# Performance work log

Hardware: AMD Instinct MI355X
Metric: run time of the kernel (lower is better)

## Reference

```python
import jax, jax.numpy as jnp
import numpy as np

B, C, H, W = 16, 256, 64, 64
NH, WS = 8, 8  # num_heads, window_size
HD = C // NH   # head_dim = 32


def setup_inputs() -> dict:
    key = jax.random.key(0)
    k1, k2, k3 = jax.random.split(key, 3)
    x = jax.random.normal(k1, (B, C, H, W), dtype=jnp.float32)
    w_qkv = jax.random.normal(k2, (3 * C, C), dtype=jnp.float32) * 0.02  # 1x1 conv, no bias
    w_proj = jax.random.normal(k3, (C, C), dtype=jnp.float32) * 0.02
    return {"x": x, "w_qkv": w_qkv, "w_proj": w_proj, "shift": 1}


def _window_partition(t, ws):
    # [b,c,h,w] -> [b*(h/ws)*(w/ws), ws*ws, c]
    b, c, h, w = t.shape
    t = t.reshape(b, c, h // ws, ws, w // ws, ws)
    t = t.transpose(0, 2, 4, 3, 5, 1)
    return t.reshape(-1, ws * ws, c)


def _window_reverse(t, b, c, h, w, ws):
    t = t.reshape(b, h // ws, w // ws, ws, ws, c)
    t = t.transpose(0, 5, 1, 3, 2, 4)
    return t.reshape(b, c, h, w)


def reference(x, w_qkv, w_proj, shift):
    b, c, h, w = x.shape
    ws = min(WS, h, w)
    shift_size = ws // 2 if (shift and ws > 1 and h % ws == 0 and w % ws == 0) else 0
    if shift_size > 0:
        x = jnp.roll(x, (-shift_size, -shift_size), axis=(2, 3))
    # 1x1 conv QKV: [b,c,h,w] x [3c,c] -> [b,3c,h,w]
    qkv = jnp.einsum('bchw,oc->bohw', x, w_qkv)
    q, k, v = jnp.split(qkv, 3, axis=1)
    q_t = _window_partition(q, ws)  # [Bw, S, c], S = ws*ws
    k_t = _window_partition(k, ws)
    v_t = _window_partition(v, ws)
    bw, s, _ = q_t.shape
    # heads: [Bw, nh, S, hd]
    qh = q_t.reshape(bw, s, NH, HD).transpose(0, 2, 1, 3)
    kh = k_t.reshape(bw, s, NH, HD).transpose(0, 2, 1, 3)
    vh = v_t.reshape(bw, s, NH, HD).transpose(0, 2, 1, 3)
    scale = 1.0 / jnp.sqrt(jnp.asarray(HD, dtype=qh.dtype))
    scores = jnp.einsum('bnqd,bnkd->bnqk', qh, kh) * scale
    attn = jax.nn.softmax(scores, axis=-1)
    out = jnp.einsum('bnqk,bnkd->bnqd', attn, vh)
    out = out.transpose(0, 2, 1, 3).reshape(bw, s, c)
    out = _window_reverse(out, b, c, h, w, ws)
    if shift_size > 0:
        out = jnp.roll(out, (shift_size, shift_size), axis=(2, 3))
    return jnp.einsum('bchw,oc->bohw', out, w_proj)
```

## Files before the change

kernel.cpp:

```cpp
#include <hip/hip_runtime.h>

typedef short bf16x8 __attribute__((ext_vector_type(8)));
typedef float f32x4 __attribute__((ext_vector_type(4)));
typedef unsigned short u16;
typedef unsigned int u32;

static __device__ __forceinline__ u16 f2bf(float f) {
  u32 u = __builtin_bit_cast(u32, f);
  u32 r = (u + 0x7FFFu + ((u >> 16) & 1u)) >> 16;
  return (u16)r;
}

__global__ __launch_bounds__(256) void k_conv(
    const float* __restrict__ wqkv, const float* __restrict__ wproj,
    u16* __restrict__ wbf) {
  const int cid = blockIdx.x * 256 + threadIdx.x;
  const float* src;
  int dst;
  if (cid < 24576) {
    const int tile = cid >> 9, rem = cid & 511;
    const int k = rem >> 6, lane = rem & 63;
    src = wqkv + (size_t)(tile * 16 + (lane & 15)) * 256 + k * 32 + (lane >> 4) * 8;
    dst = cid;
  } else {
    const int pid = cid - 24576;
    const int mt = pid >> 9, rem = pid & 511;
    const int h = rem >> 6, lane = rem & 63;
    src = wproj + (size_t)(mt * 16 + (lane & 15)) * 256 + h * 32 + (lane >> 4) * 8;
    dst = 24576 + h * 1024 + mt * 64 + lane;
  }
  float4 f0 = *(const float4*)(src);
  float4 f1 = *(const float4*)(src + 4);
  ushort4 a, b;
  a.x = f2bf(f0.x); a.y = f2bf(f0.y); a.z = f2bf(f0.z); a.w = f2bf(f0.w);
  b.x = f2bf(f1.x); b.y = f2bf(f1.y); b.z = f2bf(f1.z); b.w = f2bf(f1.w);
  *(ushort4*)(wbf + (size_t)dst * 8) = a;
  *(ushort4*)(wbf + (size_t)dst * 8 + 4) = b;
}

#define BUF0 0
#define BUF1 4096
#define XB 0
#define QH 8192
#define KH 10752
#define VTH 13312
#define PH 15616
#define LDS_TOT 20224

#define MEMF() asm volatile("" ::: "memory")
#define ENTRY()                                                      \
  do {                                                               \
    asm volatile("s_waitcnt vmcnt(0) lgkmcnt(0)" ::: "memory");      \
    __builtin_amdgcn_s_barrier();                                    \
    MEMF();                                                          \
  } while (0)

#define GL2LDS(gp, lp)                                   \
  __builtin_amdgcn_global_load_lds(                      \
      (__attribute__((address_space(1))) void*)(gp),     \
      (__attribute__((address_space(3))) void*)(lp), 16, 0, 0)

static __device__ __forceinline__ void stage_half(const u16* g, u16* l, int t) {
#pragma unroll
  for (int j = 0; j < 2; ++j) {
    const int off = (j * 256 + t) * 8;
    GL2LDS(g + off, l + off);
  }
}

#define QKV_TILE(BUFB, DSTB, U)                                           \
  do {                                                                    \
    const u16* wb_ = LDS + (BUFB) + lane * 8;                             \
    f32x4 acc = {0.f, 0.f, 0.f, 0.f};                                     \
    _Pragma("unroll") for (int k = 0; k < 8; ++k) acc =                   \
        __builtin_amdgcn_mfma_f32_16x16x32_bf16(                          \
            af[k], *(const bf16x8*)(wb_ + k * 512), acc, 0, 0, 0);        \
    _Pragma("unroll") for (int r = 0; r < 4; ++r)                         \
        LDS[(DSTB) + (pos0 + r) * 40 + (U) * 16 + l15] = f2bf(acc[r]);    \
  } while (0)

#define V_TILE(BUFB, U)                                                   \
  do {                                                                    \
    const u16* wb_ = LDS + (BUFB) + lane * 8;                             \
    f32x4 acc = {0.f, 0.f, 0.f, 0.f};                                     \
    _Pragma("unroll") for (int k = 0; k < 8; ++k) acc =                   \
        __builtin_amdgcn_mfma_f32_16x16x32_bf16(                          \
            af[k], *(const bf16x8*)(wb_ + k * 512), acc, 0, 0, 0);        \
    ushort4 pk;                                                           \
    pk.x = f2bf(acc[0]); pk.y = f2bf(acc[1]);                             \
    pk.z = f2bf(acc[2]); pk.w = f2bf(acc[3]);                             \
    *(ushort4*)&LDS[VTH + ((U) * 16 + l15) * 72 + pos0] = pk;             \
  } while (0)

__global__ __launch_bounds__(256, 4) void k_fused(
    const float* __restrict__ x, const u16* __restrict__ wbf,
    const int* __restrict__ shiftp, float* __restrict__ out) {
  __shared__ u16 LDS[LDS_TOT];
  const int blk = blockIdx.x;
  const int win = ((blk & 127) << 3) | (blk >> 7);
  const int b = win >> 6, wh = (win >> 3) & 7, ww = win & 7;
  const int off = (shiftp[0] != 0) ? 4 : 0;
  const int t = threadIdx.x;

  {
    const int slot = (blk >> 8) & 3;
    if (slot == 1) __builtin_amdgcn_s_sleep(16);
    else if (slot == 2) __builtin_amdgcn_s_sleep(32);
    else if (slot == 3) __builtin_amdgcn_s_sleep(48);
  }

  {
    u16* X = LDS + XB;
    const int wr = t & 7;
    const int h = ((wh << 3) + wr + off) & 63;
    const int w0 = ((ww << 3) + off) & 63;
    const int w1 = ((ww << 3) + off + 4) & 63;
    const int p0 = wr << 3;
#pragma unroll
    for (int it = 0; it < 8; ++it) {
      const int c = (t >> 3) + (it << 5);
      const float* src = x + ((size_t)(b * 256 + c) * 64 + h) * 64;
      float4 v0 = *(const float4*)(src + w0);
      float4 v1 = *(const float4*)(src + w1);
      X[(p0 + 0) * 264 + c] = f2bf(v0.x);
      X[(p0 + 1) * 264 + c] = f2bf(v0.y);
      X[(p0 + 2) * 264 + c] = f2bf(v0.z);
      X[(p0 + 3) * 264 + c] = f2bf(v0.w);
      X[(p0 + 4) * 264 + c] = f2bf(v1.x);
      X[(p0 + 5) * 264 + c] = f2bf(v1.y);
      X[(p0 + 6) * 264 + c] = f2bf(v1.z);
      X[(p0 + 7) * 264 + c] = f2bf(v1.w);
    }
  }
  __syncthreads();

  const int lane = t & 63, wv = t >> 6;
  const int l15 = lane & 15, quad = lane >> 4;
  const int pos0 = wv * 16 + quad * 4;

  bf16x8 af[8];
#pragma unroll
  for (int k = 0; k < 8; ++k)
    af[k] = *(const bf16x8*)&LDS[XB + (wv * 16 + l15) * 264 + quad * 8 + k * 32];
  asm volatile("s_waitcnt lgkmcnt(0)" ::: "memory");
  __builtin_amdgcn_s_barrier();
  MEMF();

  stage_half(wbf, LDS + BUF0, t);

  f32x4 accP[16];
#pragma unroll
  for (int mt = 0; mt < 16; ++mt) accP[mt] = (f32x4){0.f, 0.f, 0.f, 0.f};

  const float scale = 0.17677669529663687f;
  u16* Pw = LDS + PH + wv * 1152;
  bf16x8 bo;

#pragma unroll 1
  for (int h = 0; h < 8; ++h) {
    ENTRY();
    stage_half(wbf + (size_t)(h * 2 + 1) * 4096, LDS + BUF1, t);
    QKV_TILE(BUF0, QH, 0);
    ENTRY();
    stage_half(wbf + (size_t)(16 + h * 2) * 4096, LDS + BUF0, t);
    QKV_TILE(BUF1, QH, 1);
    ENTRY();
    stage_half(wbf + (size_t)(17 + h * 2) * 4096, LDS + BUF1, t);
    QKV_TILE(BUF0, KH, 0);
    ENTRY();
    stage_half(wbf + (size_t)(32 + h * 2) * 4096, LDS + BUF0, t);
    QKV_TILE(BUF1, KH, 1);
    ENTRY();
    stage_half(wbf + (size_t)(33 + h * 2) * 4096, LDS + BUF1, t);
    V_TILE(BUF0, 0);
    ENTRY();
    stage_half(wbf + 196608 + (size_t)h * 8192, LDS + BUF0, t);
    V_TILE(BUF1, 1);
    ENTRY();
    stage_half(wbf + 196608 + (size_t)h * 8192 + 4096, LDS + BUF1, t);
    {
      bf16x8 aq = *(const bf16x8*)&LDS[QH + (wv * 16 + l15) * 40 + quad * 8];
      f32x4 sc[4];
#pragma unroll
      for (int nt = 0; nt < 4; ++nt) {
        bf16x8 bk = *(const bf16x8*)&LDS[KH + (nt * 16 + l15) * 40 + quad * 8];
        f32x4 z = {0.f, 0.f, 0.f, 0.f};
        sc[nt] = __builtin_amdgcn_mfma_f32_16x16x32_bf16(aq, bk, z, 0, 0, 0);
      }
#pragma unroll
      for (int r = 0; r < 4; ++r) {
        float mx = -1e30f;
#pragma unroll
        for (int nt = 0; nt < 4; ++nt) mx = fmaxf(mx, sc[nt][r]);
        mx = fmaxf(mx, __shfl_xor(mx, 1));
        mx = fmaxf(mx, __shfl_xor(mx, 2));
        mx = fmaxf(mx, __shfl_xor(mx, 4));
        mx = fmaxf(mx, __shfl_xor(mx, 8));
        float p[4], sum = 0.f;
#pragma unroll
        for (int nt = 0; nt < 4; ++nt) {
          p[nt] = __expf((sc[nt][r] - mx) * scale);
          sum += p[nt];
        }
        sum += __shfl_xor(sum, 1);
        sum += __shfl_xor(sum, 2);
        sum += __shfl_xor(sum, 4);
        sum += __shfl_xor(sum, 8);
        const float is = 1.f / sum;
#pragma unroll
        for (int nt = 0; nt < 4; ++nt)
          Pw[(quad * 4 + r) * 72 + nt * 16 + l15] = f2bf(p[nt] * is);
      }
      f32x4 oa[2];
      oa[0] = (f32x4){0.f, 0.f, 0.f, 0.f};
      oa[1] = (f32x4){0.f, 0.f, 0.f, 0.f};
#pragma unroll
      for (int kk = 0; kk < 2; ++kk) {
        bf16x8 ap = *(const bf16x8*)&Pw[l15 * 72 + kk * 32 + quad * 8];
#pragma unroll
        for (int n2 = 0; n2 < 2; ++n2) {
          bf16x8 bv =
              *(const bf16x8*)&LDS[VTH + (n2 * 16 + l15) * 72 + kk * 32 + quad * 8];
          oa[n2] = __builtin_amdgcn_mfma_f32_16x16x32_bf16(ap, bv, oa[n2], 0, 0, 0);
        }
      }
#pragma unroll
      for (int n2 = 0; n2 < 2; ++n2)
#pragma unroll
        for (int r = 0; r < 4; ++r)
          LDS[QH + (pos0 + r) * 40 + n2 * 16 + l15] = f2bf(oa[n2][r]);
      bo = *(const bf16x8*)&LDS[QH + (wv * 16 + l15) * 40 + quad * 8];
#pragma unroll
      for (int mt = 0; mt < 8; ++mt) {
        bf16x8 aw = *(const bf16x8*)&LDS[BUF0 + mt * 512 + lane * 8];
        accP[mt] = __builtin_amdgcn_mfma_f32_16x16x32_bf16(aw, bo, accP[mt], 0, 0, 0);
      }
    }
    ENTRY();
    if (h < 7)
      stage_half(wbf + (size_t)((h + 1) * 2) * 4096, LDS + BUF0, t);
#pragma unroll
    for (int mt = 0; mt < 8; ++mt) {
      bf16x8 aw = *(const bf16x8*)&LDS[BUF1 + mt * 512 + lane * 8];
      accP[8 + mt] =
          __builtin_amdgcn_mfma_f32_16x16x32_bf16(aw, bo, accP[8 + mt], 0, 0, 0);
    }
  }

  const int pos = wv * 16 + l15;
  const int hco = ((wh << 3) + (pos >> 3) + off) & 63;
  const int wco = ((ww << 3) + (pos & 7) + off) & 63;
#pragma unroll
  for (int mt = 0; mt < 16; ++mt)
#pragma unroll
    for (int r = 0; r < 4; ++r) {
      const int c = mt * 16 + quad * 4 + r;
      out[((size_t)(b * 256 + c) << 12) + (hco << 6) + wco] = accP[mt][r];
    }
}

extern "C" void kernel_launch(void* const* d_in, const int* in_sizes, int n_in,
                              void* d_out, int out_size, void* d_ws, size_t ws_size,
                              hipStream_t stream) {
  const float* x = (const float*)d_in[0];
  const float* wqkv = (const float*)d_in[1];
  const float* wproj = (const float*)d_in[2];
  const int* shiftp = (const int*)d_in[3];
  float* outp = (float*)d_out;
  u16* wbf = (u16*)d_ws;
  hipLaunchKernelGGL(k_conv, dim3(128), dim3(256), 0, stream, wqkv, wproj, wbf);
  hipLaunchKernelGGL(k_fused, dim3(1024), dim3(256), 0, stream, x, wbf, shiftp, outp);
}
```

Measured before the change: 222.4 us.

## Process two windows per 512-thread block to share staged weight tiles

```diff
diff --git a/kernel.cpp b/kernel.cpp
--- a/kernel.cpp
+++ b/kernel.cpp
@@ -40,12 +40,12 @@
 
 #define BUF0 0
 #define BUF1 4096
-#define XB 0
-#define QH 8192
-#define KH 10752
-#define VTH 13312
-#define PH 15616
-#define LDS_TOT 20224
+#define ATT_BASE 8192
+#define ATT_STRIDE 12032
+#define KH_OFF 2560
+#define VTH_OFF 5120
+#define P_OFF 7424
+#define LDS_TOT 32256
 
 #define MEMF() asm volatile("" ::: "memory")
 #define ENTRY()                                                      \
@@ -60,12 +60,8 @@
       (__attribute__((address_space(1))) void*)(gp),     \
       (__attribute__((address_space(3))) void*)(lp), 16, 0, 0)
 
-static __device__ __forceinline__ void stage_half(const u16* g, u16* l, int t) {
-#pragma unroll
-  for (int j = 0; j < 2; ++j) {
-    const int off = (j * 256 + t) * 8;
-    GL2LDS(g + off, l + off);
-  }
+static __device__ __forceinline__ void stage1(const u16* g, u16* l, int t) {
+  GL2LDS(g + t * 8, l + t * 8);
 }
 
 #define QKV_TILE(BUFB, DSTB, U)                                           \
@@ -89,101 +85,105 @@
     ushort4 pk;                                                           \
     pk.x = f2bf(acc[0]); pk.y = f2bf(acc[1]);                             \
     pk.z = f2bf(acc[2]); pk.w = f2bf(acc[3]);                             \
-    *(ushort4*)&LDS[VTH + ((U) * 16 + l15) * 72 + pos0] = pk;             \
+    *(ushort4*)&LDS[VTHs + ((U) * 16 + l15) * 72 + pos0] = pk;            \
   } while (0)
 
-__global__ __launch_bounds__(256, 4) void k_fused(
+__global__ __launch_bounds__(512, 4) void k_fused(
     const float* __restrict__ x, const u16* __restrict__ wbf,
     const int* __restrict__ shiftp, float* __restrict__ out) {
   __shared__ u16 LDS[LDS_TOT];
   const int blk = blockIdx.x;
-  const int win = ((blk & 127) << 3) | (blk >> 7);
-  const int b = win >> 6, wh = (win >> 3) & 7, ww = win & 7;
+  const int pair = ((blk & 127) << 2) | (blk >> 7);
+  const int b = pair >> 5, wh = (pair >> 2) & 7, wwp = pair & 3;
   const int off = (shiftp[0] != 0) ? 4 : 0;
   const int t = threadIdx.x;
-
-  {
-    const int slot = (blk >> 8) & 3;
-    if (slot == 1) __builtin_amdgcn_s_sleep(16);
-    else if (slot == 2) __builtin_amdgcn_s_sleep(32);
-    else if (slot == 3) __builtin_amdgcn_s_sleep(48);
-  }
-
-  {
-    u16* X = LDS + XB;
-    const int wr = t & 7;
-    const int h = ((wh << 3) + wr + off) & 63;
-    const int w0 = ((ww << 3) + off) & 63;
-    const int w1 = ((ww << 3) + off + 4) & 63;
-    const int p0 = wr << 3;
-#pragma unroll
-    for (int it = 0; it < 8; ++it) {
-      const int c = (t >> 3) + (it << 5);
-      const float* src = x + ((size_t)(b * 256 + c) * 64 + h) * 64;
-      float4 v0 = *(const float4*)(src + w0);
-      float4 v1 = *(const float4*)(src + w1);
-      X[(p0 + 0) * 264 + c] = f2bf(v0.x);
-      X[(p0 + 1) * 264 + c] = f2bf(v0.y);
-      X[(p0 + 2) * 264 + c] = f2bf(v0.z);
-      X[(p0 + 3) * 264 + c] = f2bf(v0.w);
-      X[(p0 + 4) * 264 + c] = f2bf(v1.x);
-      X[(p0 + 5) * 264 + c] = f2bf(v1.y);
-      X[(p0 + 6) * 264 + c] = f2bf(v1.z);
-      X[(p0 + 7) * 264 + c] = f2bf(v1.w);
-    }
-  }
-  __syncthreads();
-
-  const int lane = t & 63, wv = t >> 6;
+  const int side = t >> 8;
+  const int ww = wwp * 2 + side;
+
+  if ((blk >> 8) & 1) __builtin_amdgcn_s_sleep(24);
+
+  const int lane = t & 63, wv = (t >> 6) & 3;
   const int l15 = lane & 15, quad = lane >> 4;
   const int pos0 = wv * 16 + quad * 4;
 
   bf16x8 af[8];
-#pragma unroll
-  for (int k = 0; k < 8; ++k)
-    af[k] = *(const bf16x8*)&LDS[XB + (wv * 16 + l15) * 264 + quad * 8 + k * 32];
-  asm volatile("s_waitcnt lgkmcnt(0)" ::: "memory");
-  __builtin_amdgcn_s_barrier();
-  MEMF();
-
-  stage_half(wbf, LDS + BUF0, t);
+#pragma unroll 1
+  for (int s = 0; s < 2; ++s) {
+    {
+      u16* X = LDS;
+      const int wr = t & 7;
+      const int h = ((wh << 3) + wr + off) & 63;
+      const int wx = wwp * 2 + s;
+      const int w0 = ((wx << 3) + off) & 63;
+      const int w1 = ((wx << 3) + off + 4) & 63;
+      const int p0 = wr << 3;
+#pragma unroll
+      for (int it = 0; it < 4; ++it) {
+        const int c = (t >> 3) + (it << 6);
+        const float* src = x + ((size_t)(b * 256 + c) * 64 + h) * 64;
+        float4 v0 = *(const float4*)(src + w0);
+        float4 v1 = *(const float4*)(src + w1);
+        X[(p0 + 0) * 264 + c] = f2bf(v0.x);
+        X[(p0 + 1) * 264 + c] = f2bf(v0.y);
+        X[(p0 + 2) * 264 + c] = f2bf(v0.z);
+        X[(p0 + 3) * 264 + c] = f2bf(v0.w);
+        X[(p0 + 4) * 264 + c] = f2bf(v1.x);
+        X[(p0 + 5) * 264 + c] = f2bf(v1.y);
+        X[(p0 + 6) * 264 + c] = f2bf(v1.z);
+        X[(p0 + 7) * 264 + c] = f2bf(v1.w);
+      }
+    }
+    __syncthreads();
+    if (side == s) {
+#pragma unroll
+      for (int k = 0; k < 8; ++k)
+        af[k] = *(const bf16x8*)&LDS[(wv * 16 + l15) * 264 + quad * 8 + k * 32];
+    }
+    asm volatile("s_waitcnt lgkmcnt(0)" ::: "memory");
+    __syncthreads();
+  }
+
+  stage1(wbf, LDS + BUF0, t);
+
+  const int AT = ATT_BASE + side * ATT_STRIDE;
+  const int QHs = AT, KHs = AT + KH_OFF, VTHs = AT + VTH_OFF;
+  u16* Pw = LDS + AT + P_OFF + wv * 1152;
 
   f32x4 accP[16];
 #pragma unroll
   for (int mt = 0; mt < 16; ++mt) accP[mt] = (f32x4){0.f, 0.f, 0.f, 0.f};
 
   const float scale = 0.17677669529663687f;
-  u16* Pw = LDS + PH + wv * 1152;
   bf16x8 bo;
 
 #pragma unroll 1
   for (int h = 0; h < 8; ++h) {
     ENTRY();
-    stage_half(wbf + (size_t)(h * 2 + 1) * 4096, LDS + BUF1, t);
-    QKV_TILE(BUF0, QH, 0);
-    ENTRY();
-    stage_half(wbf + (size_t)(16 + h * 2) * 4096, LDS + BUF0, t);
-    QKV_TILE(BUF1, QH, 1);
-    ENTRY();
-    stage_half(wbf + (size_t)(17 + h * 2) * 4096, LDS + BUF1, t);
-    QKV_TILE(BUF0, KH, 0);
-    ENTRY();
-    stage_half(wbf + (size_t)(32 + h * 2) * 4096, LDS + BUF0, t);
-    QKV_TILE(BUF1, KH, 1);
-    ENTRY();
-    stage_half(wbf + (size_t)(33 + h * 2) * 4096, LDS + BUF1, t);
+    stage1(wbf + (size_t)(h * 2 + 1) * 4096, LDS + BUF1, t);
+    QKV_TILE(BUF0, QHs, 0);
+    ENTRY();
+    stage1(wbf + (size_t)(16 + h * 2) * 4096, LDS + BUF0, t);
+    QKV_TILE(BUF1, QHs, 1);
+    ENTRY();
+    stage1(wbf + (size_t)(17 + h * 2) * 4096, LDS + BUF1, t);
+    QKV_TILE(BUF0, KHs, 0);
+    ENTRY();
+    stage1(wbf + (size_t)(32 + h * 2) * 4096, LDS + BUF0, t);
+    QKV_TILE(BUF1, KHs, 1);
+    ENTRY();
+    stage1(wbf + (size_t)(33 + h * 2) * 4096, LDS + BUF1, t);
     V_TILE(BUF0, 0);
     ENTRY();
-    stage_half(wbf + 196608 + (size_t)h * 8192, LDS + BUF0, t);
+    stage1(wbf + 196608 + (size_t)h * 8192, LDS + BUF0, t);
     V_TILE(BUF1, 1);
     ENTRY();
-    stage_half(wbf + 196608 + (size_t)h * 8192 + 4096, LDS + BUF1, t);
+    stage1(wbf + 196608 + (size_t)h * 8192 + 4096, LDS + BUF1, t);
     {
-      bf16x8 aq = *(const bf16x8*)&LDS[QH + (wv * 16 + l15) * 40 + quad * 8];
+      bf16x8 aq = *(const bf16x8*)&LDS[QHs + (wv * 16 + l15) * 40 + quad * 8];
       f32x4 sc[4];
 #pragma unroll
       for (int nt = 0; nt < 4; ++nt) {
-        bf16x8 bk = *(const bf16x8*)&LDS[KH + (nt * 16 + l15) * 40 + quad * 8];
+        bf16x8 bk = *(const bf16x8*)&LDS[KHs + (nt * 16 + l15) * 40 + quad * 8];
         f32x4 z = {0.f, 0.f, 0.f, 0.f};
         sc[nt] = __builtin_amdgcn_mfma_f32_16x16x32_bf16(aq, bk, z, 0, 0, 0);
       }
@@ -220,7 +220,7 @@
 #pragma unroll
         for (int n2 = 0; n2 < 2; ++n2) {
           bf16x8 bv =
-              *(const bf16x8*)&LDS[VTH + (n2 * 16 + l15) * 72 + kk * 32 + quad * 8];
+              *(const bf16x8*)&LDS[VTHs + (n2 * 16 + l15) * 72 + kk * 32 + quad * 8];
           oa[n2] = __builtin_amdgcn_mfma_f32_16x16x32_bf16(ap, bv, oa[n2], 0, 0, 0);
         }
       }
@@ -228,8 +228,8 @@
       for (int n2 = 0; n2 < 2; ++n2)
 #pragma unroll
         for (int r = 0; r < 4; ++r)
-          LDS[QH + (pos0 + r) * 40 + n2 * 16 + l15] = f2bf(oa[n2][r]);
-      bo = *(const bf16x8*)&LDS[QH + (wv * 16 + l15) * 40 + quad * 8];
+          LDS[QHs + (pos0 + r) * 40 + n2 * 16 + l15] = f2bf(oa[n2][r]);
+      bo = *(const bf16x8*)&LDS[QHs + (wv * 16 + l15) * 40 + quad * 8];
 #pragma unroll
       for (int mt = 0; mt < 8; ++mt) {
         bf16x8 aw = *(const bf16x8*)&LDS[BUF0 + mt * 512 + lane * 8];
@@ -238,7 +238,7 @@
     }
     ENTRY();
     if (h < 7)
-      stage_half(wbf + (size_t)((h + 1) * 2) * 4096, LDS + BUF0, t);
+      stage1(wbf + (size_t)((h + 1) * 2) * 4096, LDS + BUF0, t);
 #pragma unroll
     for (int mt = 0; mt < 8; ++mt) {
       bf16x8 aw = *(const bf16x8*)&LDS[BUF1 + mt * 512 + lane * 8];
@@ -269,5 +269,5 @@
   float* outp = (float*)d_out;
   u16* wbf = (u16*)d_ws;
   hipLaunchKernelGGL(k_conv, dim3(128), dim3(256), 0, stream, wqkv, wproj, wbf);
-  hipLaunchKernelGGL(k_fused, dim3(1024), dim3(256), 0, stream, x, wbf, shiftp, outp);
-}
+  hipLaunchKernelGGL(k_fused, dim3(512), dim3(512), 0, stream, x, wbf, shiftp, outp);
+}
```

New measurement: 228.9 us. 1.03x slower.

## Split QKV and projection GEMMs across wave pairs with 4-buffer weight staging

Applied to the files above, without the earlier changes.

```diff
diff --git a/kernel.cpp b/kernel.cpp
--- a/kernel.cpp
+++ b/kernel.cpp
@@ -38,22 +38,30 @@
   *(ushort4*)(wbf + (size_t)dst * 8 + 4) = b;
 }
 
-#define BUF0 0
-#define BUF1 4096
-#define XB 0
-#define QH 8192
-#define KH 10752
-#define VTH 13312
-#define PH 15616
-#define LDS_TOT 20224
+#define B0 0
+#define B1 4096
+#define B2 8192
+#define B3 12288
+#define QH 16384
+#define KH 18944
+#define VTH 21504
+#define PH 23808
+#define LDS_TOT 28416
 
 #define MEMF() asm volatile("" ::: "memory")
+#define BAR()                        \
+  do {                               \
+    MEMF();                          \
+    __builtin_amdgcn_s_barrier();    \
+    MEMF();                          \
+  } while (0)
 #define ENTRY()                                                      \
   do {                                                               \
     asm volatile("s_waitcnt vmcnt(0) lgkmcnt(0)" ::: "memory");      \
     __builtin_amdgcn_s_barrier();                                    \
     MEMF();                                                          \
   } while (0)
+#define WLG0() asm volatile("s_waitcnt lgkmcnt(0)" ::: "memory")
 
 #define GL2LDS(gp, lp)                                   \
   __builtin_amdgcn_global_load_lds(                      \
@@ -68,31 +76,43 @@
   }
 }
 
-#define QKV_TILE(BUFB, DSTB, U)                                           \
-  do {                                                                    \
-    const u16* wb_ = LDS + (BUFB) + lane * 8;                             \
-    f32x4 acc = {0.f, 0.f, 0.f, 0.f};                                     \
-    _Pragma("unroll") for (int k = 0; k < 8; ++k) acc =                   \
-        __builtin_amdgcn_mfma_f32_16x16x32_bf16(                          \
-            af[k], *(const bf16x8*)(wb_ + k * 512), acc, 0, 0, 0);        \
-    _Pragma("unroll") for (int r = 0; r < 4; ++r)                         \
-        LDS[(DSTB) + (pos0 + r) * 40 + (U) * 16 + l15] = f2bf(acc[r]);    \
+#define GEMM_TILE(BUFB, DSTB, U)                                              \
+  do {                                                                        \
+    const u16* wb_ = LDS + (BUFB) + lane * 8;                                 \
+    f32x4 a0 = {0.f, 0.f, 0.f, 0.f}, a1 = {0.f, 0.f, 0.f, 0.f};               \
+    _Pragma("unroll") for (int k = 0; k < 8; ++k) {                           \
+      const bf16x8 bf_ = *(const bf16x8*)(wb_ + k * 512);                     \
+      a0 = __builtin_amdgcn_mfma_f32_16x16x32_bf16(af0[k], bf_, a0, 0, 0, 0); \
+      a1 = __builtin_amdgcn_mfma_f32_16x16x32_bf16(af1[k], bf_, a1, 0, 0, 0); \
+    }                                                                         \
+    _Pragma("unroll") for (int r = 0; r < 4; ++r) {                           \
+      LDS[(DSTB) + (wp * 32 + quad * 4 + r) * 40 + (U) * 16 + l15] =          \
+          f2bf(a0[r]);                                                        \
+      LDS[(DSTB) + (wp * 32 + 16 + quad * 4 + r) * 40 + (U) * 16 + l15] =     \
+          f2bf(a1[r]);                                                        \
+    }                                                                         \
   } while (0)
 
-#define V_TILE(BUFB, U)                                                   \
-  do {                                                                    \
-    const u16* wb_ = LDS + (BUFB) + lane * 8;                             \
-    f32x4 acc = {0.f, 0.f, 0.f, 0.f};                                     \
-    _Pragma("unroll") for (int k = 0; k < 8; ++k) acc =                   \
-        __builtin_amdgcn_mfma_f32_16x16x32_bf16(                          \
-            af[k], *(const bf16x8*)(wb_ + k * 512), acc, 0, 0, 0);        \
-    ushort4 pk;                                                           \
-    pk.x = f2bf(acc[0]); pk.y = f2bf(acc[1]);                             \
-    pk.z = f2bf(acc[2]); pk.w = f2bf(acc[3]);                             \
-    *(ushort4*)&LDS[VTH + ((U) * 16 + l15) * 72 + pos0] = pk;             \
+#define VGEMM_TILE(BUFB, U)                                                   \
+  do {                                                                        \
+    const u16* wb_ = LDS + (BUFB) + lane * 8;                                 \
+    f32x4 a0 = {0.f, 0.f, 0.f, 0.f}, a1 = {0.f, 0.f, 0.f, 0.f};               \
+    _Pragma("unroll") for (int k = 0; k < 8; ++k) {                           \
+      const bf16x8 bf_ = *(const bf16x8*)(wb_ + k * 512);                     \
+      a0 = __builtin_amdgcn_mfma_f32_16x16x32_bf16(af0[k], bf_, a0, 0, 0, 0); \
+      a1 = __builtin_amdgcn_mfma_f32_16x16x32_bf16(af1[k], bf_, a1, 0, 0, 0); \
+    }                                                                         \
+    ushort4 pk0, pk1;                                                         \
+    pk0.x = f2bf(a0[0]); pk0.y = f2bf(a0[1]);                                 \
+    pk0.z = f2bf(a0[2]); pk0.w = f2bf(a0[3]);                                 \
+    pk1.x = f2bf(a1[0]); pk1.y = f2bf(a1[1]);                                 \
+    pk1.z = f2bf(a1[2]); pk1.w = f2bf(a1[3]);                                 \
+    *(ushort4*)&LDS[VTH + ((U) * 16 + l15) * 72 + wp * 32 + quad * 4] = pk0;  \
+    *(ushort4*)&LDS[VTH + ((U) * 16 + l15) * 72 + wp * 32 + 16 + quad * 4] =  \
+        pk1;                                                                  \
   } while (0)
 
-__global__ __launch_bounds__(256, 4) void k_fused(
+__global__ __launch_bounds__(256, 2) void k_fused(
     const float* __restrict__ x, const u16* __restrict__ wbf,
     const int* __restrict__ shiftp, float* __restrict__ out) {
   __shared__ u16 LDS[LDS_TOT];
@@ -110,7 +130,7 @@
   }
 
   {
-    u16* X = LDS + XB;
+    u16* X = LDS;
     const int wr = t & 7;
     const int h = ((wh << 3) + wr + off) & 63;
     const int w0 = ((ww << 3) + off) & 63;
@@ -136,48 +156,54 @@
 
   const int lane = t & 63, wv = t >> 6;
   const int l15 = lane & 15, quad = lane >> 4;
-  const int pos0 = wv * 16 + quad * 4;
-
-  bf16x8 af[8];
-#pragma unroll
-  for (int k = 0; k < 8; ++k)
-    af[k] = *(const bf16x8*)&LDS[XB + (wv * 16 + l15) * 264 + quad * 8 + k * 32];
-  asm volatile("s_waitcnt lgkmcnt(0)" ::: "memory");
-  __builtin_amdgcn_s_barrier();
-  MEMF();
-
-  stage_half(wbf, LDS + BUF0, t);
-
-  f32x4 accP[16];
-#pragma unroll
-  for (int mt = 0; mt < 16; ++mt) accP[mt] = (f32x4){0.f, 0.f, 0.f, 0.f};
+  const int wp = wv >> 1, wc = wv & 1;
+  const int apos0 = wv * 16 + quad * 4;
+
+  bf16x8 af0[8], af1[8];
+#pragma unroll
+  for (int k = 0; k < 8; ++k) {
+    af0[k] = *(const bf16x8*)&LDS[(wp * 32 + l15) * 264 + quad * 8 + k * 32];
+    af1[k] =
+        *(const bf16x8*)&LDS[(wp * 32 + 16 + l15) * 264 + quad * 8 + k * 32];
+  }
+  WLG0();
+  BAR();
+
+  stage_half(wbf, LDS + B0, t);
+  stage_half(wbf + (size_t)17 * 4096, LDS + B1, t);
+
+  f32x4 accP[8][2];
+#pragma unroll
+  for (int mt = 0; mt < 8; ++mt) {
+    accP[mt][0] = (f32x4){0.f, 0.f, 0.f, 0.f};
+    accP[mt][1] = (f32x4){0.f, 0.f, 0.f, 0.f};
+  }
 
   const float scale = 0.17677669529663687f;
   u16* Pw = LDS + PH + wv * 1152;
-  bf16x8 bo;
 
 #pragma unroll 1
   for (int h = 0; h < 8; ++h) {
     ENTRY();
-    stage_half(wbf + (size_t)(h * 2 + 1) * 4096, LDS + BUF1, t);
-    QKV_TILE(BUF0, QH, 0);
+    stage_half(wbf + (size_t)(h * 2 + 1) * 4096, LDS + B2, t);
+    stage_half(wbf + (size_t)(32 + h * 2) * 4096, LDS + B3, t);
+    if (wc == 0) GEMM_TILE(B0, QH, 0);
+    else GEMM_TILE(B1, KH, 1);
     ENTRY();
-    stage_half(wbf + (size_t)(16 + h * 2) * 4096, LDS + BUF0, t);
-    QKV_TILE(BUF1, QH, 1);
+    stage_half(wbf + (size_t)(16 + h * 2) * 4096, LDS + B0, t);
+    stage_half(wbf + (size_t)(33 + h * 2) * 4096, LDS + B1, t);
+    if (wc == 0) GEMM_TILE(B2, QH, 1);
+    else VGEMM_TILE(B3, 0);
     ENTRY();
-    stage_half(wbf + (size_t)(17 + h * 2) * 4096, LDS + BUF1, t);
-    QKV_TILE(BUF0, KH, 0);
+    stage_half(wbf + 196608 + (size_t)h * 8192, LDS + B2, t);
+    stage_half(wbf + 196608 + (size_t)h * 8192 + 4096, LDS + B3, t);
+    if (wc == 0) GEMM_TILE(B0, KH, 0);
+    else VGEMM_TILE(B1, 1);
     ENTRY();
-    stage_half(wbf + (size_t)(32 + h * 2) * 4096, LDS + BUF0, t);
-    QKV_TILE(BUF1, KH, 1);
-    ENTRY();
-    stage_half(wbf + (size_t)(33 + h * 2) * 4096, LDS + BUF1, t);
-    V_TILE(BUF0, 0);
-    ENTRY();
-    stage_half(wbf + 196608 + (size_t)h * 8192, LDS + BUF0, t);
-    V_TILE(BUF1, 1);
-    ENTRY();
-    stage_half(wbf + 196608 + (size_t)h * 8192 + 4096, LDS + BUF1, t);
+    if (h < 7) {
+      stage_half(wbf + (size_t)((h + 1) * 2) * 4096, LDS + B0, t);
+      stage_half(wbf + (size_t)(17 + (h + 1) * 2) * 4096, LDS + B1, t);
+    }
     {
       bf16x8 aq = *(const bf16x8*)&LDS[QH + (wv * 16 + l15) * 40 + quad * 8];
       f32x4 sc[4];
@@ -219,8 +245,8 @@
         bf16x8 ap = *(const bf16x8*)&Pw[l15 * 72 + kk * 32 + quad * 8];
 #pragma unroll
         for (int n2 = 0; n2 < 2; ++n2) {
-          bf16x8 bv =
-              *(const bf16x8*)&LDS[VTH + (n2 * 16 + l15) * 72 + kk * 32 + quad * 8];
+          bf16x8 bv = *(const bf16x8*)&LDS[VTH + (n2 * 16 + l15) * 72 +
+                                           kk * 32 + quad * 8];
           oa[n2] = __builtin_amdgcn_mfma_f32_16x16x32_bf16(ap, bv, oa[n2], 0, 0, 0);
         }
       }
@@ -228,35 +254,40 @@
       for (int n2 = 0; n2 < 2; ++n2)
 #pragma unroll
         for (int r = 0; r < 4; ++r)
-          LDS[QH + (pos0 + r) * 40 + n2 * 16 + l15] = f2bf(oa[n2][r]);
-      bo = *(const bf16x8*)&LDS[QH + (wv * 16 + l15) * 40 + quad * 8];
+          LDS[QH + (apos0 + r) * 40 + n2 * 16 + l15] = f2bf(oa[n2][r]);
+    }
+    WLG0();
+    BAR();
+    {
+      const int pjb = (wc == 0) ? B2 : B3;
+      bf16x8 bo0 =
+          *(const bf16x8*)&LDS[QH + (wp * 32 + l15) * 40 + quad * 8];
+      bf16x8 bo1 =
+          *(const bf16x8*)&LDS[QH + (wp * 32 + 16 + l15) * 40 + quad * 8];
 #pragma unroll
       for (int mt = 0; mt < 8; ++mt) {
-        bf16x8 aw = *(const bf16x8*)&LDS[BUF0 + mt * 512 + lane * 8];
-        accP[mt] = __builtin_amdgcn_mfma_f32_16x16x32_bf16(aw, bo, accP[mt], 0, 0, 0);
+        bf16x8 aw = *(const bf16x8*)&LDS[pjb + mt * 512 + lane * 8];
+        accP[mt][0] =
+            __builtin_amdgcn_mfma_f32_16x16x32_bf16(aw, bo0, accP[mt][0], 0, 0, 0);
+        accP[mt][1] =
+            __builtin_amdgcn_mfma_f32_16x16x32_bf16(aw, bo1, accP[mt][1], 0, 0, 0);
       }
     }
-    ENTRY();
-    if (h < 7)
-      stage_half(wbf + (size_t)((h + 1) * 2) * 4096, LDS + BUF0, t);
-#pragma unroll
-    for (int mt = 0; mt < 8; ++mt) {
-      bf16x8 aw = *(const bf16x8*)&LDS[BUF1 + mt * 512 + lane * 8];
-      accP[8 + mt] =
-          __builtin_amdgcn_mfma_f32_16x16x32_bf16(aw, bo, accP[8 + mt], 0, 0, 0);
-    }
-  }
-
-  const int pos = wv * 16 + l15;
-  const int hco = ((wh << 3) + (pos >> 3) + off) & 63;
-  const int wco = ((ww << 3) + (pos & 7) + off) & 63;
-#pragma unroll
-  for (int mt = 0; mt < 16; ++mt)
-#pragma unroll
-    for (int r = 0; r < 4; ++r) {
-      const int c = mt * 16 + quad * 4 + r;
-      out[((size_t)(b * 256 + c) << 12) + (hco << 6) + wco] = accP[mt][r];
-    }
+  }
+
+#pragma unroll
+  for (int i = 0; i < 2; ++i) {
+    const int pos = wp * 32 + i * 16 + l15;
+    const int hco = ((wh << 3) + (pos >> 3) + off) & 63;
+    const int wco = ((ww << 3) + (pos & 7) + off) & 63;
+#pragma unroll
+    for (int mt = 0; mt < 8; ++mt)
+#pragma unroll
+      for (int r = 0; r < 4; ++r) {
+        const int c = wc * 128 + mt * 16 + quad * 4 + r;
+        out[((size_t)(b * 256 + c) << 12) + (hco << 6) + wco] = accP[mt][i][r];
+      }
+  }
 }
 
 extern "C" void kernel_launch(void* const* d_in, const int* in_sizes, int n_in,
```

New measurement: 221.6 us. About the same (-0.4%).
